# Performance work log

Measured on AMD Instinct MI355X. Metric: run time of the kernel, lower is better.

## Reference

```python
import jax, jax.numpy as jnp
import numpy as np

TOKENS = 8192
IN_F = 4096
OUT_F = 4096
QMAX = 127.0  # int8 symmetric quant range
EPS = 1e-8


def setup_inputs() -> dict:
    key = jax.random.key(0)
    k1, k2, k3, k4 = jax.random.split(key, 4)
    x = jax.random.normal(k1, (TOKENS, IN_F), dtype=jnp.float32)
    # Pre-quantized int8 weight [out_features, in_features]
    weight_q = jax.random.randint(k2, (OUT_F, IN_F), -127, 128, dtype=jnp.int8)
    # Per-output-channel weight scales (realistic small magnitudes)
    weight_scale = jax.random.uniform(k3, (OUT_F,), dtype=jnp.float32) * 0.01 + 1e-3
    bias = jax.random.normal(k4, (OUT_F,), dtype=jnp.float32)
    return {"x": x, "weight_q": weight_q, "weight_scale": weight_scale, "bias": bias}


def reference(x, weight_q, weight_scale, bias):
    # Dynamic per-token symmetric int8 activation quantization
    absmax = jnp.max(jnp.abs(x), axis=-1, keepdims=True)           # [T, 1]
    x_scale = jnp.maximum(absmax, EPS) / QMAX                      # [T, 1]
    x_q = jnp.clip(jnp.round(x / x_scale), -QMAX, QMAX).astype(jnp.int8)
    acc = jax.lax.dot_general(
        x_q, weight_q,
        dimension_numbers=(((1,), (1,)), ((), ())),
        preferred_element_type=jnp.int32,
    )
    # Inline dequant: per-token activation scale * per-channel weight scale
    out = acc.astype(jnp.float32) * x_scale * weight_scale[None, :]
    out = out + bias[None, :]
    return out
```

## Files before the change

### kernel.cpp

```cpp
#include <hip/hip_runtime.h>
#include <cstdint>
#include <cstddef>

#define TOKENS 8192
#define IN_F   4096
#define OUT_F  4096
#define QMAXF  127.0f
#define EPSF   1e-8f

typedef int i32x4  __attribute__((ext_vector_type(4)));
typedef int i32x16 __attribute__((ext_vector_type(16)));

#define BKB 64
#define NT  (IN_F / BKB)
#define LDS_BUF   32768
#define LDS_TOTAL (3 * LDS_BUF)

__device__ __forceinline__ void gload16(const void* g, void* l) {
    __builtin_amdgcn_global_load_lds(
        (const __attribute__((address_space(1))) void*)g,
        (__attribute__((address_space(3))) void*)l,
        16, 0, 0);
}

__device__ __forceinline__ void bar() {
    asm volatile("" ::: "memory");
    __builtin_amdgcn_s_barrier();
    asm volatile("" ::: "memory");
}

__device__ __forceinline__ int quant1(float v, float inv) {
    int q = (int)rintf(v * inv);
    q = q > 127 ? 127 : q;
    q = q < -127 ? -127 : q;
    return q;
}

__device__ __forceinline__ unsigned int pack4i(int a, int b, int c, int d) {
    return (unsigned int)(a & 255) | ((unsigned int)(b & 255) << 8) |
           ((unsigned int)(c & 255) << 16) | ((unsigned int)(d & 255) << 24);
}

__global__ __launch_bounds__(256) void quant_x_kernel(const float* __restrict__ x,
                                                      signed char* __restrict__ xq,
                                                      float* __restrict__ xscale) {
    const int t   = blockIdx.x;
    const int tid = threadIdx.x;
    const float* xr = x + (size_t)t * IN_F + tid * 16;

    float4 v[4];
    float am = 0.0f;
#pragma unroll
    for (int i = 0; i < 4; ++i) {
        v[i] = ((const float4*)xr)[i];
        am = fmaxf(am, fmaxf(fmaxf(fabsf(v[i].x), fabsf(v[i].y)),
                             fmaxf(fabsf(v[i].z), fabsf(v[i].w))));
    }
#pragma unroll
    for (int off = 32; off >= 1; off >>= 1)
        am = fmaxf(am, __shfl_xor(am, off));

    __shared__ float wmax[4];
    const int wid = tid >> 6, lane = tid & 63;
    if (lane == 0) wmax[wid] = am;
    __syncthreads();
    am = fmaxf(fmaxf(wmax[0], wmax[1]), fmaxf(wmax[2], wmax[3]));

    const float s   = fmaxf(am, EPSF) / QMAXF;
    const float inv = QMAXF / fmaxf(am, EPSF);
    if (tid == 0) xscale[t] = s;

    unsigned int w[4];
#pragma unroll
    for (int i = 0; i < 4; ++i) {
        w[i] = pack4i(quant1(v[i].x, inv), quant1(v[i].y, inv),
                      quant1(v[i].z, inv), quant1(v[i].w, inv));
    }
    *(uint4*)(xq + (size_t)t * IN_F + tid * 16) = make_uint4(w[0], w[1], w[2], w[3]);
}

__global__ __launch_bounds__(256) void pack_w_kernel(const int* __restrict__ w,
                                                     signed char* __restrict__ wq) {
    const size_t idx = (size_t)blockIdx.x * 256 + threadIdx.x;
    const int4* src = (const int4*)w + idx * 4;
    unsigned int o[4];
#pragma unroll
    for (int i = 0; i < 4; ++i) {
        int4 u = src[i];
        o[i] = pack4i(u.x, u.y, u.z, u.w);
    }
    ((uint4*)wq)[idx] = make_uint4(o[0], o[1], o[2], o[3]);
}

__global__ __launch_bounds__(512, 2) void gemm_kernel(const signed char* __restrict__ xq,
                                                      const signed char* __restrict__ wq,
                                                      const float* __restrict__ xscale,
                                                      const float* __restrict__ wscale,
                                                      const float* __restrict__ bias,
                                                      float* __restrict__ out) {
    extern __shared__ __align__(16) char lds[];

    const int tid  = threadIdx.x;
    const int wid  = tid >> 6;
    const int lane = tid & 63;
    const int wr   = wid >> 2;
    const int wc   = wid & 3;
    const int bid  = blockIdx.x;
    const int bm0  = (bid & 31) * 256;
    const int bn0  = (bid >> 5) * 256;

    const int srow = (tid >> 6) * 16 + (tid & 15);
    const int scol = ((tid >> 4) & 3) * 16;
    const signed char* gA0 = xq + (size_t)(bm0 + srow)       * IN_F + scol;
    const signed char* gA1 = xq + (size_t)(bm0 + 128 + srow) * IN_F + scol;
    const signed char* gB0 = wq + (size_t)(bn0 + srow)       * IN_F + scol;
    const signed char* gB1 = wq + (size_t)(bn0 + 128 + srow) * IN_F + scol;
    const int ldst = tid * 16;

    const int l31 = lane & 31, hi = lane >> 5;
    int a_off[4][2], b_off[2][2];
#pragma unroll
    for (int m = 0; m < 4; ++m) {
        const int rw = wr * 8 + m * 2 + (l31 >> 4);
        const int rb = (l31 & 15) * 16;
#pragma unroll
        for (int ks = 0; ks < 2; ++ks)
            a_off[m][ks] = rw * 1024 + (ks * 2 + hi) * 256 + rb;
    }
#pragma unroll
    for (int n = 0; n < 2; ++n) {
        const int rw = wc * 4 + n * 2 + (l31 >> 4);
        const int rb = (l31 & 15) * 16;
#pragma unroll
        for (int ks = 0; ks < 2; ++ks)
            b_off[n][ks] = 16384 + rw * 1024 + (ks * 2 + hi) * 256 + rb;
    }

    i32x16 acc[4][2];
#pragma unroll
    for (int m = 0; m < 4; ++m)
#pragma unroll
        for (int n = 0; n < 2; ++n)
#pragma unroll
            for (int r = 0; r < 16; ++r) acc[m][n][r] = 0;

    {
        char* S0 = lds;
        gload16(gA0,       S0 + ldst);
        gload16(gA1,       S0 + 8192  + ldst);
        gload16(gB0,       S0 + 16384 + ldst);
        gload16(gB1,       S0 + 24576 + ldst);
        char* S1 = lds + LDS_BUF;
        gload16(gA0 + BKB, S1 + ldst);
        gload16(gA1 + BKB, S1 + 8192  + ldst);
        gload16(gB0 + BKB, S1 + 16384 + ldst);
        gload16(gB1 + BKB, S1 + 24576 + ldst);
    }
    asm volatile("s_waitcnt vmcnt(4)" ::: "memory");
    bar();

    int cur = 0, nxt = 2;
    for (int t = 0; t < NT; ++t) {
        const char* Ab = lds + cur * LDS_BUF;
        char* Sd = lds + nxt * LDS_BUF;
        const bool st = (t + 2 < NT);
        const int koff = (t + 2) * BKB;

        i32x4 a0[4], b0[2];
#pragma unroll
        for (int m = 0; m < 4; ++m) a0[m] = *(const i32x4*)(Ab + a_off[m][0]);
#pragma unroll
        for (int n = 0; n < 2; ++n) b0[n] = *(const i32x4*)(Ab + b_off[n][0]);
        if (st) {
            gload16(gA0 + koff, Sd + ldst);
            gload16(gB0 + koff, Sd + 16384 + ldst);
        }
        bar();
        __builtin_amdgcn_s_setprio(1);
#pragma unroll
        for (int m = 0; m < 4; ++m)
#pragma unroll
            for (int n = 0; n < 2; ++n)
                acc[m][n] = __builtin_amdgcn_mfma_i32_32x32x32_i8(a0[m], b0[n], acc[m][n], 0, 0, 0);
        __builtin_amdgcn_s_setprio(0);
        bar();

        i32x4 a1[4], b1[2];
#pragma unroll
        for (int m = 0; m < 4; ++m) a1[m] = *(const i32x4*)(Ab + a_off[m][1]);
#pragma unroll
        for (int n = 0; n < 2; ++n) b1[n] = *(const i32x4*)(Ab + b_off[n][1]);
        if (st) {
            gload16(gA1 + koff, Sd + 8192  + ldst);
            gload16(gB1 + koff, Sd + 24576 + ldst);
        }
        bar();
        __builtin_amdgcn_s_setprio(1);
#pragma unroll
        for (int m = 0; m < 4; ++m)
#pragma unroll
            for (int n = 0; n < 2; ++n)
                acc[m][n] = __builtin_amdgcn_mfma_i32_32x32x32_i8(a1[m], b1[n], acc[m][n], 0, 0, 0);
        __builtin_amdgcn_s_setprio(0);

        if (t + 2 < NT) {
            asm volatile("s_waitcnt vmcnt(4)" ::: "memory");
        } else if (t + 1 < NT) {
            asm volatile("s_waitcnt vmcnt(0)" ::: "memory");
        }
        bar();

        cur = (cur == 2) ? 0 : cur + 1;
        nxt = (nxt == 2) ? 0 : nxt + 1;
    }

#pragma unroll
    for (int m = 0; m < 4; ++m) {
        const int rbase = bm0 + wr * 128 + m * 32 + 4 * hi;
        float xsv[16];
#pragma unroll
        for (int r = 0; r < 16; ++r)
            xsv[r] = xscale[rbase + (r & 3) + 8 * (r >> 2)];
#pragma unroll
        for (int n = 0; n < 2; ++n) {
            const int col = bn0 + wc * 64 + n * 32 + l31;
            const float wsc = wscale[col];
            const float bv  = bias[col];
#pragma unroll
            for (int r = 0; r < 16; ++r) {
                const int row = rbase + (r & 3) + 8 * (r >> 2);
                out[(size_t)row * OUT_F + col] = (float)acc[m][n][r] * xsv[r] * wsc + bv;
            }
        }
    }
}

extern "C" void kernel_launch(void* const* d_in, const int* in_sizes, int n_in,
                              void* d_out, int out_size, void* d_ws, size_t ws_size,
                              hipStream_t stream) {
    const float* x      = (const float*)d_in[0];
    const int*   w      = (const int*)d_in[1];
    const float* wscale = (const float*)d_in[2];
    const float* bias   = (const float*)d_in[3];
    float* out = (float*)d_out;

    char* ws = (char*)d_ws;
    signed char* xq  = (signed char*)ws;
    signed char* wq8 = (signed char*)(ws + (size_t)TOKENS * IN_F);
    float* xscale    = (float*)(ws + (size_t)TOKENS * IN_F + (size_t)OUT_F * IN_F);

    hipFuncSetAttribute((const void*)gemm_kernel,
                        hipFuncAttributeMaxDynamicSharedMemorySize, LDS_TOTAL);

    quant_x_kernel<<<TOKENS, 256, 0, stream>>>(x, xq, xscale);
    pack_w_kernel<<<(OUT_F * (IN_F / 16)) / 256, 256, 0, stream>>>(w, wq8);
    gemm_kernel<<<(TOKENS / 256) * (OUT_F / 256), 512, LDS_TOTAL, stream>>>(
        xq, wq8, xscale, wscale, bias, out);
}
```

Measured before the change: 205.4 us.

## Deepen LDS pipeline to four buffers and prefetch next tile into registers

```diff
diff --git a/kernel.cpp b/kernel.cpp
--- a/kernel.cpp
+++ b/kernel.cpp
@@ -14,7 +14,8 @@
 #define BKB 64
 #define NT  (IN_F / BKB)
 #define LDS_BUF   32768
-#define LDS_TOTAL (3 * LDS_BUF)
+#define NBUF 4
+#define LDS_TOTAL (NBUF * LDS_BUF)
 
 __device__ __forceinline__ void gload16(const void* g, void* l) {
     __builtin_amdgcn_global_load_lds(
@@ -144,38 +145,40 @@
 #pragma unroll
             for (int r = 0; r < 16; ++r) acc[m][n][r] = 0;
 
-    {
-        char* S0 = lds;
-        gload16(gA0,       S0 + ldst);
-        gload16(gA1,       S0 + 8192  + ldst);
-        gload16(gB0,       S0 + 16384 + ldst);
-        gload16(gB1,       S0 + 24576 + ldst);
-        char* S1 = lds + LDS_BUF;
-        gload16(gA0 + BKB, S1 + ldst);
-        gload16(gA1 + BKB, S1 + 8192  + ldst);
-        gload16(gB0 + BKB, S1 + 16384 + ldst);
-        gload16(gB1 + BKB, S1 + 24576 + ldst);
+#pragma unroll
+    for (int s = 0; s < 3; ++s) {
+        char* S = lds + s * LDS_BUF;
+        const int ko = s * BKB;
+        gload16(gA0 + ko, S + ldst);
+        gload16(gA1 + ko, S + 8192  + ldst);
+        gload16(gB0 + ko, S + 16384 + ldst);
+        gload16(gB1 + ko, S + 24576 + ldst);
     }
     asm volatile("s_waitcnt vmcnt(4)" ::: "memory");
     bar();
 
-    int cur = 0, nxt = 2;
+    i32x4 a0[4], b0[2];
+#pragma unroll
+    for (int m = 0; m < 4; ++m) a0[m] = *(const i32x4*)(lds + a_off[m][0]);
+#pragma unroll
+    for (int n = 0; n < 2; ++n) b0[n] = *(const i32x4*)(lds + b_off[n][0]);
+
     for (int t = 0; t < NT; ++t) {
-        const char* Ab = lds + cur * LDS_BUF;
-        char* Sd = lds + nxt * LDS_BUF;
-        const bool st = (t + 2 < NT);
-        const int koff = (t + 2) * BKB;
-
-        i32x4 a0[4], b0[2];
-#pragma unroll
-        for (int m = 0; m < 4; ++m) a0[m] = *(const i32x4*)(Ab + a_off[m][0]);
-#pragma unroll
-        for (int n = 0; n < 2; ++n) b0[n] = *(const i32x4*)(Ab + b_off[n][0]);
+        const char* Ab = lds + (t & 3) * LDS_BUF;
+        const char* An = lds + ((t + 1) & 3) * LDS_BUF;
+        char* Sd = lds + ((t + 3) & 3) * LDS_BUF;
+        const bool st = (t + 3 < NT);
+        const int koff = (t + 3) * BKB;
+
+        i32x4 a1[4], b1[2];
+#pragma unroll
+        for (int m = 0; m < 4; ++m) a1[m] = *(const i32x4*)(Ab + a_off[m][1]);
+#pragma unroll
+        for (int n = 0; n < 2; ++n) b1[n] = *(const i32x4*)(Ab + b_off[n][1]);
         if (st) {
             gload16(gA0 + koff, Sd + ldst);
             gload16(gB0 + koff, Sd + 16384 + ldst);
         }
-        bar();
         __builtin_amdgcn_s_setprio(1);
 #pragma unroll
         for (int m = 0; m < 4; ++m)
@@ -183,18 +186,16 @@
             for (int n = 0; n < 2; ++n)
                 acc[m][n] = __builtin_amdgcn_mfma_i32_32x32x32_i8(a0[m], b0[n], acc[m][n], 0, 0, 0);
         __builtin_amdgcn_s_setprio(0);
-        bar();
-
-        i32x4 a1[4], b1[2];
-#pragma unroll
-        for (int m = 0; m < 4; ++m) a1[m] = *(const i32x4*)(Ab + a_off[m][1]);
-#pragma unroll
-        for (int n = 0; n < 2; ++n) b1[n] = *(const i32x4*)(Ab + b_off[n][1]);
+
+        i32x4 a0n[4], b0n[2];
+#pragma unroll
+        for (int m = 0; m < 4; ++m) a0n[m] = *(const i32x4*)(An + a_off[m][0]);
+#pragma unroll
+        for (int n = 0; n < 2; ++n) b0n[n] = *(const i32x4*)(An + b_off[n][0]);
         if (st) {
             gload16(gA1 + koff, Sd + 8192  + ldst);
             gload16(gB1 + koff, Sd + 24576 + ldst);
         }
-        bar();
         __builtin_amdgcn_s_setprio(1);
 #pragma unroll
         for (int m = 0; m < 4; ++m)
@@ -203,15 +204,17 @@
                 acc[m][n] = __builtin_amdgcn_mfma_i32_32x32x32_i8(a1[m], b1[n], acc[m][n], 0, 0, 0);
         __builtin_amdgcn_s_setprio(0);
 
-        if (t + 2 < NT) {
+        if (t + 3 < NT) {
             asm volatile("s_waitcnt vmcnt(4)" ::: "memory");
-        } else if (t + 1 < NT) {
+        } else {
             asm volatile("s_waitcnt vmcnt(0)" ::: "memory");
         }
         bar();
 
-        cur = (cur == 2) ? 0 : cur + 1;
-        nxt = (nxt == 2) ? 0 : nxt + 1;
+#pragma unroll
+        for (int m = 0; m < 4; ++m) a0[m] = a0n[m];
+#pragma unroll
+        for (int n = 0; n < 2; ++n) b0[n] = b0n[n];
     }
 
 #pragma unroll
```

Result: no change. 208.9 us (+1.7%).
